# Kernel tuning notes

Hardware: AMD Instinct MI355X
Metric: run time of the kernel (lower is better)

The kernel has to match this reference:

```python
import jax, jax.numpy as jnp
import numpy as np

D_MODEL = 2048
N_HEAD = 32
N_KV_HEAD = 8
N_REP = N_HEAD // N_KV_HEAD
D_K = D_MODEL // N_HEAD
THETA = 10000.0
B, S = 2, 1024


def setup_inputs() -> dict:
    key = jax.random.key(0)
    ks = jax.random.split(key, 9)
    sd = 1.0 / np.sqrt(D_MODEL)
    return {
        "x": jax.random.normal(ks[0], (B, S, D_MODEL), jnp.float32),
        "Wq": jax.random.normal(ks[1], (D_MODEL, D_MODEL), jnp.float32) * sd,
        "bq": jax.random.normal(ks[2], (D_MODEL,), jnp.float32) * 0.02,
        "Wk": jax.random.normal(ks[3], (D_MODEL, N_KV_HEAD * D_K), jnp.float32) * sd,
        "bk": jax.random.normal(ks[4], (N_KV_HEAD * D_K,), jnp.float32) * 0.02,
        "Wv": jax.random.normal(ks[5], (D_MODEL, N_KV_HEAD * D_K), jnp.float32) * sd,
        "bv": jax.random.normal(ks[6], (N_KV_HEAD * D_K,), jnp.float32) * 0.02,
        "Wo": jax.random.normal(ks[7], (D_MODEL, D_MODEL), jnp.float32) * sd,
        "bo": jax.random.normal(ks[8], (D_MODEL,), jnp.float32) * 0.02,
    }


def _apply_rope(t, pos):
    # t: [b, h, s, d_k], pos: [s]
    half = D_K // 2
    inv_freq = 1.0 / (THETA ** (jnp.arange(half, dtype=jnp.float32) * 2.0 / D_K))
    ang = pos[:, None].astype(jnp.float32) * inv_freq[None, :]  # [s, half]
    cos = jnp.cos(ang)[None, None]  # [1,1,s,half]
    sin = jnp.sin(ang)[None, None]
    te = t[..., 0::2]
    to = t[..., 1::2]
    re = te * cos - to * sin
    ro = te * sin + to * cos
    return jnp.stack([re, ro], axis=-1).reshape(t.shape)


def reference(x, Wq, bq, Wk, bk, Wv, bv, Wo, bo):
    b, s, _ = x.shape
    q = (x @ Wq + bq).reshape(b, s, N_HEAD, D_K).transpose(0, 2, 1, 3)
    k = (x @ Wk + bk).reshape(b, s, N_KV_HEAD, D_K).transpose(0, 2, 1, 3)
    v = (x @ Wv + bv).reshape(b, s, N_KV_HEAD, D_K).transpose(0, 2, 1, 3)
    pos = jnp.arange(s)
    q = _apply_rope(q, pos)
    k = _apply_rope(k, pos)
    # GQA head repeat: [b, n_kv, s, d] -> [b, n_head, s, d]
    k = jnp.repeat(k, N_REP, axis=1)
    v = jnp.repeat(v, N_REP, axis=1)
    scores = jnp.einsum('bhnd,bhmd->bhnm', q, k) / jnp.sqrt(jnp.float32(D_K))
    mask = jnp.tril(jnp.ones((s, s), dtype=bool))
    scores = jnp.where(mask[None, None], scores, jnp.float32(-jnp.inf))
    probs = jax.nn.softmax(scores, axis=-1)
    out = jnp.einsum('bhnm,bhmd->bhnd', probs, v)
    out = out.transpose(0, 2, 1, 3).reshape(b, s, D_MODEL)
    return out @ Wo + bo
```

## Files before the change

kernel.cpp:

```cpp
#include <hip/hip_runtime.h>
#include <hip/hip_bf16.h>

#define D_MODEL 2048
#define N_HEAD 32
#define N_KV_HEAD 8
#define N_REP 4
#define D_K 64
#define S_LEN 1024
#define B_SZ 2
#define M_ROWS (B_SZ * S_LEN)
#define KV_DIM (N_KV_HEAD * D_K)
#define QKV_N 3072
#define KOFF 2048
#define VOFF 2560
#define LOG2E 1.44269504088896f

typedef __attribute__((ext_vector_type(8))) short short8;
typedef __attribute__((ext_vector_type(4))) float f32x4;

#define EXP2F(x) __builtin_amdgcn_exp2f(x)

__device__ inline unsigned short f2bf(float f) {
    union { float f; unsigned int u; } x{f};
    unsigned int r = x.u + 0x7fffu + ((x.u >> 16) & 1u);
    return (unsigned short)(r >> 16);
}
__device__ inline float bf2f(unsigned short b) {
    union { unsigned int u; float f; } x; x.u = ((unsigned int)b) << 16; return x.f;
}
__device__ inline void store_c(float* p, float v) { *p = v; }
__device__ inline void store_c(unsigned short* p, float v) { *p = f2bf(v); }

__device__ inline void load_lds16(const unsigned short* g, unsigned short* l) {
    __builtin_amdgcn_global_load_lds(
        (const __attribute__((address_space(1))) unsigned int*)g,
        (__attribute__((address_space(3))) unsigned int*)l, 16, 0, 0);
}

__global__ __launch_bounds__(256) void wprep_kernel(
        const float* __restrict__ Wq_, const float* __restrict__ Wk_,
        const float* __restrict__ Wv_, const float* __restrict__ Wo_,
        unsigned short* __restrict__ WtQKV, unsigned short* __restrict__ WtO) {
    const float* src; unsigned short* dst; int N;
    switch (blockIdx.z) {
        case 0: src = Wq_; dst = WtQKV; N = D_MODEL; break;
        case 1: src = Wk_; dst = WtQKV + (size_t)KOFF * D_MODEL; N = KV_DIM; break;
        case 2: src = Wv_; dst = WtQKV + (size_t)VOFF * D_MODEL; N = KV_DIM; break;
        default: src = Wo_; dst = WtO; N = D_MODEL; break;
    }
    int n0 = blockIdx.x * 64;
    if (n0 >= N) return;
    int k0 = blockIdx.y * 64;
    int t = threadIdx.x;
    int n = n0 + (t >> 2);
    int ks = k0 + (t & 3) * 16;
    unsigned int pk[8];
#pragma unroll
    for (int i = 0; i < 8; i++) {
        float a = src[(size_t)(ks + 2 * i) * N + n];
        float b = src[(size_t)(ks + 2 * i + 1) * N + n];
        pk[i] = (unsigned int)f2bf(a) | ((unsigned int)f2bf(b) << 16);
    }
    uint4* d = (uint4*)&dst[(size_t)n * D_MODEL + ks];
    d[0] = make_uint4(pk[0], pk[1], pk[2], pk[3]);
    d[1] = make_uint4(pk[4], pk[5], pk[6], pk[7]);
}

__global__ void cast_bf_kernel(const float* __restrict__ src,
                               unsigned short* __restrict__ dst, int n4) {
    int idx = blockIdx.x * blockDim.x + threadIdx.x;
    if (idx >= n4) return;
    float4 v = ((const float4*)src)[idx];
    unsigned int lo = (unsigned int)f2bf(v.x) | ((unsigned int)f2bf(v.y) << 16);
    unsigned int hi = (unsigned int)f2bf(v.z) | ((unsigned int)f2bf(v.w) << 16);
    ((uint2*)dst)[idx] = make_uint2(lo, hi);
}

__global__ void concat_bias_kernel(const float* __restrict__ bq, const float* __restrict__ bk,
                                   const float* __restrict__ bv, float* __restrict__ dst) {
    int i = blockIdx.x * blockDim.x + threadIdx.x;
    if (i >= QKV_N) return;
    dst[i] = (i < KOFF) ? bq[i] : (i < VOFF) ? bk[i - KOFF] : bv[i - VOFF];
}

template <typename TC>
__global__ __launch_bounds__(256) void gemm_bf16_kernel(
        const unsigned short* __restrict__ A,
        const unsigned short* __restrict__ Bt,
        const float* __restrict__ bias,
        TC* __restrict__ C, int M, int N, int K) {
    __shared__ unsigned short As[128 * 64];
    __shared__ unsigned short Bs[64 * 64];
    const int tid = threadIdx.x, lane = tid & 63;
    const int w = tid >> 6, wm = w >> 1, wn = w & 1;
    const int quad = lane >> 4, lr = lane & 15;
    const int bm = blockIdx.y * 128, bn = blockIdx.x * 64;

    f32x4 acc[4][2];
#pragma unroll
    for (int i = 0; i < 4; i++)
#pragma unroll
        for (int j = 0; j < 2; j++) acc[i][j] = (f32x4){0.f, 0.f, 0.f, 0.f};

    for (int k0 = 0; k0 < K; k0 += 64) {
        __syncthreads();
#pragma unroll
        for (int it = 0; it < 4; it++) {
            int slot = it * 256 + tid;
            int row = slot >> 3;
            int qc = (slot & 7) ^ (row & 7);
            load_lds16(A + (size_t)(bm + row) * K + k0 + qc * 8, &As[slot * 8]);
        }
#pragma unroll
        for (int it = 0; it < 2; it++) {
            int slot = it * 256 + tid;
            int row = slot >> 3;
            int qc = (slot & 7) ^ (row & 7);
            load_lds16(Bt + (size_t)(bn + row) * K + k0 + qc * 8, &Bs[slot * 8]);
        }
        __syncthreads();
#pragma unroll
        for (int ks = 0; ks < 2; ks++) {
            short8 af[4], bf[2];
#pragma unroll
            for (int i = 0; i < 4; i++) {
                int row = wm * 64 + i * 16 + lr;
                af[i] = *(const short8*)&As[(row * 8 + ((ks * 4 + quad) ^ (lr & 7))) * 8];
            }
#pragma unroll
            for (int j = 0; j < 2; j++) {
                int row = wn * 32 + j * 16 + lr;
                bf[j] = *(const short8*)&Bs[(row * 8 + ((ks * 4 + quad) ^ (lr & 7))) * 8];
            }
#pragma unroll
            for (int i = 0; i < 4; i++)
#pragma unroll
                for (int j = 0; j < 2; j++)
                    acc[i][j] = __builtin_amdgcn_mfma_f32_16x16x32_bf16(af[i], bf[j], acc[i][j], 0, 0, 0);
        }
    }
#pragma unroll
    for (int i = 0; i < 4; i++) {
#pragma unroll
        for (int j = 0; j < 2; j++) {
            int col = bn + wn * 32 + j * 16 + lr;
            int row0 = bm + wm * 64 + i * 16 + quad * 4;
            float bj = bias[col];
#pragma unroll
            for (int r = 0; r < 4; r++)
                store_c(&C[(size_t)(row0 + r) * N + col], acc[i][j][r] + bj);
        }
    }
}

__global__ void rope_bf_kernel(unsigned short* __restrict__ t) {
    const int QI = M_ROWS * N_HEAD * 32;
    const int TOT = QI + M_ROWS * N_KV_HEAD * 32;
    int idx = blockIdx.x * blockDim.x + threadIdx.x;
    if (idx >= TOT) return;
    int col_off, n_heads;
    float scale;
    if (idx < QI) { col_off = 0; n_heads = N_HEAD; scale = 0.125f * LOG2E; }
    else { idx -= QI; col_off = KOFF; n_heads = N_KV_HEAD; scale = 1.0f; }
    int i = idx & 31;
    int hh = (idx >> 5) % n_heads;
    int r = idx / (32 * n_heads);
    int s = r % S_LEN;
    float inv_freq = EXP2F((float)i * -0.41524101186f);
    float ang = (float)s * inv_freq;
    float c = __cosf(ang), sn = __sinf(ang);
    unsigned short* p = t + (size_t)r * QKV_N + col_off + hh * D_K + 2 * i;
    float te = bf2f(p[0]), to = bf2f(p[1]);
    p[0] = f2bf((te * c - to * sn) * scale);
    p[1] = f2bf((te * sn + to * c) * scale);
}

#define AST 72
struct Pre { uint4 k0, k1, v0, v1; };

__device__ __forceinline__ void issue_pre(const unsigned short* kb,
                                          const unsigned short* vb,
                                          int j0, int tid, Pre& p) {
    int f0 = tid, f1 = tid + 256;
    p.k0 = *(const uint4*)(kb + (size_t)(j0 + (f0 >> 3)) * QKV_N + (f0 & 7) * 8);
    p.k1 = *(const uint4*)(kb + (size_t)(j0 + (f1 >> 3)) * QKV_N + (f1 & 7) * 8);
    int kp = tid & 31, dg = tid >> 5;
    p.v0 = *(const uint4*)(vb + (size_t)(j0 + 2 * kp) * QKV_N + dg * 8);
    p.v1 = *(const uint4*)(vb + (size_t)(j0 + 2 * kp + 1) * QKV_N + dg * 8);
}
__device__ __forceinline__ void commit_pre(unsigned short* Ks, unsigned short* Vt,
                                           int tid, const Pre& p) {
    int f0 = tid, f1 = tid + 256;
    *(uint4*)&Ks[(f0 >> 3) * AST + (f0 & 7) * 8] = p.k0;
    *(uint4*)&Ks[(f1 >> 3) * AST + (f1 & 7) * 8] = p.k1;
    int kp = tid & 31, dg = tid >> 5;
    const unsigned short* ta = (const unsigned short*)&p.v0;
    const unsigned short* tb = (const unsigned short*)&p.v1;
#pragma unroll
    for (int i = 0; i < 8; i++) {
        unsigned int pk = (unsigned int)ta[i] | ((unsigned int)tb[i] << 16);
        *(unsigned int*)&Vt[(dg * 8 + i) * AST + 2 * kp] = pk;
    }
}

__device__ __forceinline__ void attn_tile(
        int w, int quad, int lr, bool diag,
        const unsigned short* Ks, const unsigned short* Vt, unsigned short* Ps,
        const short8* aq, f32x4* oacc, float* mrow, float* lrow) {
    f32x4 s[4];
#pragma unroll
    for (int cf = 0; cf < 4; cf++) s[cf] = (f32x4){0.f, 0.f, 0.f, 0.f};
#pragma unroll
    for (int ks = 0; ks < 2; ks++) {
#pragma unroll
        for (int cf = 0; cf < 4; cf++) {
            short8 bk = *(const short8*)&Ks[(cf * 16 + lr) * AST + ks * 32 + quad * 8];
            s[cf] = __builtin_amdgcn_mfma_f32_16x16x32_bf16(aq[ks], bk, s[cf], 0, 0, 0);
        }
    }
    if (diag) {
#pragma unroll
        for (int cf = 0; cf < 4; cf++) {
            int key = cf * 16 + lr;
#pragma unroll
            for (int r = 0; r < 4; r++)
                if (key > w * 16 + quad * 4 + r) s[cf][r] = -1e30f;
        }
    }
    float corr[4];
#pragma unroll
    for (int r = 0; r < 4; r++) {
        float rm = fmaxf(fmaxf(s[0][r], s[1][r]), fmaxf(s[2][r], s[3][r]));
        rm = fmaxf(rm, __shfl_xor(rm, 1));
        rm = fmaxf(rm, __shfl_xor(rm, 2));
        rm = fmaxf(rm, __shfl_xor(rm, 4));
        rm = fmaxf(rm, __shfl_xor(rm, 8));
        float mn = fmaxf(mrow[r], rm);
        corr[r] = EXP2F(mrow[r] - mn);
        mrow[r] = mn;
        float rs = 0.f;
#pragma unroll
        for (int cf = 0; cf < 4; cf++) {
            float p = EXP2F(s[cf][r] - mn);
            union { float f; unsigned int u; } px{p};
            px.u &= 0xFFFF0000u;
            Ps[(w * 16 + quad * 4 + r) * AST + cf * 16 + lr] =
                (unsigned short)(px.u >> 16);
            rs += px.f;
        }
        rs += __shfl_xor(rs, 1);
        rs += __shfl_xor(rs, 2);
        rs += __shfl_xor(rs, 4);
        rs += __shfl_xor(rs, 8);
        lrow[r] = lrow[r] * corr[r] + rs;
    }
#pragma unroll
    for (int cf = 0; cf < 4; cf++)
#pragma unroll
        for (int r = 0; r < 4; r++) oacc[cf][r] *= corr[r];
#pragma unroll
    for (int ks = 0; ks < 2; ks++) {
        short8 ap = *(const short8*)&Ps[(w * 16 + lr) * AST + ks * 32 + quad * 8];
#pragma unroll
        for (int cf = 0; cf < 4; cf++) {
            short8 bv = *(const short8*)&Vt[(cf * 16 + lr) * AST + ks * 32 + quad * 8];
            oacc[cf] = __builtin_amdgcn_mfma_f32_16x16x32_bf16(ap, bv, oacc[cf], 0, 0, 0);
        }
    }
}

__global__ __launch_bounds__(256) void attn_mfma_kernel(
        const unsigned short* __restrict__ qkv,
        unsigned short* __restrict__ obf) {
    __shared__ unsigned short Ks[64 * AST];
    __shared__ unsigned short Vt[64 * AST];
    __shared__ unsigned short Ps[64 * AST];
    const int tid = threadIdx.x;
    const int w = tid >> 6, lane = tid & 63;
    const int lr = lane & 15, quad = lane >> 4;
    const int h = blockIdx.y, b = blockIdx.z;
    const int kvh = h >> 2;
    const unsigned short* kb = qkv + (size_t)(b * S_LEN) * QKV_N + KOFF + kvh * D_K;
    const unsigned short* vb = qkv + (size_t)(b * S_LEN) * QKV_N + VOFF + kvh * D_K;

    const int qt = (h & 16) ? (15 - blockIdx.x) : blockIdx.x;
    const int nt = qt + 1;

    short8 aq[2];
    {
        const unsigned short* qp = qkv + (size_t)(b * S_LEN + qt * 64 + w * 16 + lr) * QKV_N
                                   + h * D_K + quad * 8;
        aq[0] = *(const short8*)qp;
        aq[1] = *(const short8*)(qp + 32);
    }
    f32x4 oacc[4];
#pragma unroll
    for (int cf = 0; cf < 4; cf++) oacc[cf] = (f32x4){0.f, 0.f, 0.f, 0.f};
    float m[4] = {-1e30f, -1e30f, -1e30f, -1e30f}, l[4] = {0.f, 0.f, 0.f, 0.f};

    Pre pre;
    issue_pre(kb, vb, 0, tid, pre);
    for (int t = 0; t < nt; t++) {
        __syncthreads();
        commit_pre(Ks, Vt, tid, pre);
        __syncthreads();
        if (t + 1 < nt) issue_pre(kb, vb, (t + 1) * 64, tid, pre);
        attn_tile(w, quad, lr, t == qt, Ks, Vt, Ps, aq, oacc, m, l);
    }
#pragma unroll
    for (int r = 0; r < 4; r++) {
        float inv = 1.f / l[r];
        int row = b * S_LEN + qt * 64 + w * 16 + quad * 4 + r;
#pragma unroll
        for (int cf = 0; cf < 4; cf++)
            obf[(size_t)row * D_MODEL + h * D_K + cf * 16 + lr] = f2bf(oacc[cf][r] * inv);
    }
}

extern "C" void kernel_launch(void* const* d_in, const int* in_sizes, int n_in,
                              void* d_out, int out_size, void* d_ws, size_t ws_size,
                              hipStream_t stream) {
    const float* x  = (const float*)d_in[0];
    const float* Wq = (const float*)d_in[1];
    const float* bq = (const float*)d_in[2];
    const float* Wk = (const float*)d_in[3];
    const float* bk = (const float*)d_in[4];
    const float* Wv = (const float*)d_in[5];
    const float* bv = (const float*)d_in[6];
    const float* Wo = (const float*)d_in[7];
    const float* bo = (const float*)d_in[8];
    float* out = (float*)d_out;

    unsigned short* xbf   = (unsigned short*)d_ws;
    unsigned short* WtQKV = xbf + (size_t)M_ROWS * D_MODEL;
    unsigned short* WtO   = WtQKV + (size_t)QKV_N * D_MODEL;
    unsigned short* qkv   = WtO + (size_t)D_MODEL * D_MODEL;
    float* bias_qkv       = (float*)(qkv + (size_t)M_ROWS * QKV_N);
    unsigned short* obf   = xbf;

    dim3 gb(256);

    cast_bf_kernel<<<(M_ROWS * D_MODEL / 4 + 255) / 256, gb, 0, stream>>>(x, xbf, M_ROWS * D_MODEL / 4);
    wprep_kernel<<<dim3(32, 32, 4), gb, 0, stream>>>(Wq, Wk, Wv, Wo, WtQKV, WtO);
    concat_bias_kernel<<<(QKV_N + 255) / 256, gb, 0, stream>>>(bq, bk, bv, bias_qkv);
    gemm_bf16_kernel<unsigned short><<<dim3(QKV_N / 64, M_ROWS / 128), gb, 0, stream>>>(
        xbf, WtQKV, bias_qkv, qkv, M_ROWS, QKV_N, D_MODEL);
    rope_bf_kernel<<<(M_ROWS * (N_HEAD + N_KV_HEAD) * 32 + 255) / 256, gb, 0, stream>>>(qkv);
    attn_mfma_kernel<<<dim3(16, N_HEAD, B_SZ), gb, 0, stream>>>(qkv, obf);
    gemm_bf16_kernel<float><<<dim3(D_MODEL / 64, M_ROWS / 128), gb, 0, stream>>>(
        obf, WtO, bo, out, M_ROWS, D_MODEL, D_MODEL);
}
```

Baseline: 234.6 us.

## Rewrite attention with 32x32x16 MFMA and register-resident P via permlane32 swaps

The attention kernel now uses 128-row query tiles (32 rows per wave) and 32x32x16 bf16 MFMAs. It computes S^T so each lane owns a single query row, which lets the softmax reductions work in registers with one permlane32 swap. P is repacked into MFMA operands with perm/permlane32_swap instead of a trip through LDS, which drops the Ps buffer. The output is staged through LDS for coalesced 16-byte stores. Waves in a block now see different causal extents, so some waves sit idle while others finish. The grid halves to 8x32x2 blocks with a batch-based tile-order flip, which lowers parallelism.

```diff
diff --git a/kernel.cpp b/kernel.cpp
--- a/kernel.cpp
+++ b/kernel.cpp
@@ -17,6 +17,7 @@
 
 typedef __attribute__((ext_vector_type(8))) short short8;
 typedef __attribute__((ext_vector_type(4))) float f32x4;
+typedef __attribute__((ext_vector_type(16))) float f32x16;
 
 #define EXP2F(x) __builtin_amdgcn_exp2f(x)
 
@@ -35,6 +36,11 @@
     __builtin_amdgcn_global_load_lds(
         (const __attribute__((address_space(1))) unsigned int*)g,
         (__attribute__((address_space(3))) unsigned int*)l, 16, 0, 0);
+}
+
+__device__ __forceinline__ unsigned int permpack(float hi_f, float lo_f) {
+    union { float f; unsigned int u; } a{hi_f}, b{lo_f};
+    return __builtin_amdgcn_perm(a.u, b.u, 0x07060302u);
 }
 
 __global__ __launch_bounds__(256) void wprep_kernel(
@@ -203,100 +209,38 @@
     }
 }
 
-__device__ __forceinline__ void attn_tile(
-        int w, int quad, int lr, bool diag,
-        const unsigned short* Ks, const unsigned short* Vt, unsigned short* Ps,
-        const short8* aq, f32x4* oacc, float* mrow, float* lrow) {
-    f32x4 s[4];
-#pragma unroll
-    for (int cf = 0; cf < 4; cf++) s[cf] = (f32x4){0.f, 0.f, 0.f, 0.f};
-#pragma unroll
-    for (int ks = 0; ks < 2; ks++) {
-#pragma unroll
-        for (int cf = 0; cf < 4; cf++) {
-            short8 bk = *(const short8*)&Ks[(cf * 16 + lr) * AST + ks * 32 + quad * 8];
-            s[cf] = __builtin_amdgcn_mfma_f32_16x16x32_bf16(aq[ks], bk, s[cf], 0, 0, 0);
-        }
-    }
-    if (diag) {
-#pragma unroll
-        for (int cf = 0; cf < 4; cf++) {
-            int key = cf * 16 + lr;
-#pragma unroll
-            for (int r = 0; r < 4; r++)
-                if (key > w * 16 + quad * 4 + r) s[cf][r] = -1e30f;
-        }
-    }
-    float corr[4];
-#pragma unroll
-    for (int r = 0; r < 4; r++) {
-        float rm = fmaxf(fmaxf(s[0][r], s[1][r]), fmaxf(s[2][r], s[3][r]));
-        rm = fmaxf(rm, __shfl_xor(rm, 1));
-        rm = fmaxf(rm, __shfl_xor(rm, 2));
-        rm = fmaxf(rm, __shfl_xor(rm, 4));
-        rm = fmaxf(rm, __shfl_xor(rm, 8));
-        float mn = fmaxf(mrow[r], rm);
-        corr[r] = EXP2F(mrow[r] - mn);
-        mrow[r] = mn;
-        float rs = 0.f;
-#pragma unroll
-        for (int cf = 0; cf < 4; cf++) {
-            float p = EXP2F(s[cf][r] - mn);
-            union { float f; unsigned int u; } px{p};
-            px.u &= 0xFFFF0000u;
-            Ps[(w * 16 + quad * 4 + r) * AST + cf * 16 + lr] =
-                (unsigned short)(px.u >> 16);
-            rs += px.f;
-        }
-        rs += __shfl_xor(rs, 1);
-        rs += __shfl_xor(rs, 2);
-        rs += __shfl_xor(rs, 4);
-        rs += __shfl_xor(rs, 8);
-        lrow[r] = lrow[r] * corr[r] + rs;
-    }
-#pragma unroll
-    for (int cf = 0; cf < 4; cf++)
-#pragma unroll
-        for (int r = 0; r < 4; r++) oacc[cf][r] *= corr[r];
-#pragma unroll
-    for (int ks = 0; ks < 2; ks++) {
-        short8 ap = *(const short8*)&Ps[(w * 16 + lr) * AST + ks * 32 + quad * 8];
-#pragma unroll
-        for (int cf = 0; cf < 4; cf++) {
-            short8 bv = *(const short8*)&Vt[(cf * 16 + lr) * AST + ks * 32 + quad * 8];
-            oacc[cf] = __builtin_amdgcn_mfma_f32_16x16x32_bf16(ap, bv, oacc[cf], 0, 0, 0);
-        }
-    }
-}
-
 __global__ __launch_bounds__(256) void attn_mfma_kernel(
         const unsigned short* __restrict__ qkv,
         unsigned short* __restrict__ obf) {
-    __shared__ unsigned short Ks[64 * AST];
-    __shared__ unsigned short Vt[64 * AST];
-    __shared__ unsigned short Ps[64 * AST];
+    __shared__ unsigned short SM[2 * 64 * AST];
+    unsigned short* Ks = SM;
+    unsigned short* Vt = SM + 64 * AST;
     const int tid = threadIdx.x;
     const int w = tid >> 6, lane = tid & 63;
-    const int lr = lane & 15, quad = lane >> 4;
+    const int lq = lane & 31, hi = lane >> 5;
+    const int hi8 = hi * 8, hi4 = hi * 4;
     const int h = blockIdx.y, b = blockIdx.z;
     const int kvh = h >> 2;
     const unsigned short* kb = qkv + (size_t)(b * S_LEN) * QKV_N + KOFF + kvh * D_K;
     const unsigned short* vb = qkv + (size_t)(b * S_LEN) * QKV_N + VOFF + kvh * D_K;
 
-    const int qt = (h & 16) ? (15 - blockIdx.x) : blockIdx.x;
-    const int nt = qt + 1;
-
-    short8 aq[2];
+    const int qt = b ? 7 - (int)blockIdx.x : (int)blockIdx.x;
+    const int nt = 2 * qt + 2;
+    const int qw0 = qt * 128 + w * 32;
+    const int qg = qw0 + lq;
+
+    short8 aq[4];
     {
-        const unsigned short* qp = qkv + (size_t)(b * S_LEN + qt * 64 + w * 16 + lr) * QKV_N
-                                   + h * D_K + quad * 8;
-        aq[0] = *(const short8*)qp;
-        aq[1] = *(const short8*)(qp + 32);
-    }
-    f32x4 oacc[4];
-#pragma unroll
-    for (int cf = 0; cf < 4; cf++) oacc[cf] = (f32x4){0.f, 0.f, 0.f, 0.f};
-    float m[4] = {-1e30f, -1e30f, -1e30f, -1e30f}, l[4] = {0.f, 0.f, 0.f, 0.f};
+        const unsigned short* qp = qkv + (size_t)(b * S_LEN + qg) * QKV_N + h * D_K + hi8;
+#pragma unroll
+        for (int st = 0; st < 4; st++) aq[st] = *(const short8*)(qp + st * 16);
+    }
+    f32x16 oacc[2];
+#pragma unroll
+    for (int dt = 0; dt < 2; dt++)
+#pragma unroll
+        for (int r = 0; r < 16; r++) oacc[dt][r] = 0.f;
+    float m = -1e30f, l = 0.f;
 
     Pre pre;
     issue_pre(kb, vb, 0, tid, pre);
@@ -305,15 +249,119 @@
         commit_pre(Ks, Vt, tid, pre);
         __syncthreads();
         if (t + 1 < nt) issue_pre(kb, vb, (t + 1) * 64, tid, pre);
-        attn_tile(w, quad, lr, t == qt, Ks, Vt, Ps, aq, oacc, m, l);
-    }
-#pragma unroll
-    for (int r = 0; r < 4; r++) {
-        float inv = 1.f / l[r];
-        int row = b * S_LEN + qt * 64 + w * 16 + quad * 4 + r;
-#pragma unroll
-        for (int cf = 0; cf < 4; cf++)
-            obf[(size_t)row * D_MODEL + h * D_K + cf * 16 + lr] = f2bf(oacc[cf][r] * inv);
+        const int t64 = t * 64;
+        if (t64 > qw0 + 31) continue;
+
+        f32x16 s0, s1;
+#pragma unroll
+        for (int r = 0; r < 16; r++) { s0[r] = 0.f; s1[r] = 0.f; }
+#pragma unroll
+        for (int st = 0; st < 4; st++) {
+            short8 k0 = *(const short8*)&Ks[lq * AST + st * 16 + hi8];
+            short8 k1 = *(const short8*)&Ks[(32 + lq) * AST + st * 16 + hi8];
+            s0 = __builtin_amdgcn_mfma_f32_32x32x16_bf16(k0, aq[st], s0, 0, 0, 0);
+            s1 = __builtin_amdgcn_mfma_f32_32x32x16_bf16(k1, aq[st], s1, 0, 0, 0);
+        }
+        float px[32];
+#pragma unroll
+        for (int r = 0; r < 16; r++) { px[r] = s0[r]; px[16 + r] = s1[r]; }
+        if (t64 + 63 > qw0) {
+#pragma unroll
+            for (int kh = 0; kh < 2; kh++)
+#pragma unroll
+                for (int r = 0; r < 16; r++) {
+                    int kg = t64 + kh * 32 + ((r & 3) + 8 * (r >> 2)) + hi4;
+                    if (kg > qg) px[kh * 16 + r] = -1e30f;
+                }
+        }
+        float tm[16];
+#pragma unroll
+        for (int i = 0; i < 16; i++) tm[i] = fmaxf(px[i], px[i + 16]);
+#pragma unroll
+        for (int i = 0; i < 8; i++) tm[i] = fmaxf(tm[i], tm[i + 8]);
+#pragma unroll
+        for (int i = 0; i < 4; i++) tm[i] = fmaxf(tm[i], tm[i + 4]);
+        float lmax = fmaxf(fmaxf(tm[0], tm[1]), fmaxf(tm[2], tm[3]));
+        union { float f; unsigned int u; } mb{lmax};
+        auto rr = __builtin_amdgcn_permlane32_swap((int)mb.u, (int)mb.u, false, false);
+        union { unsigned int u; float f; } ra, rb;
+        ra.u = (unsigned int)rr[0];
+        rb.u = (unsigned int)rr[1];
+        float mn = fmaxf(m, fmaxf(ra.f, rb.f));
+        float corr = EXP2F(m - mn);
+        m = mn;
+        float p[32], pm[32];
+#pragma unroll
+        for (int i = 0; i < 32; i++) {
+            p[i] = EXP2F(px[i] - mn);
+            union { float f; unsigned int u; } pu{p[i]};
+            pu.u &= 0xFFFF0000u;
+            pm[i] = pu.f;
+        }
+        float ts[16];
+#pragma unroll
+        for (int i = 0; i < 16; i++) ts[i] = pm[i] + pm[i + 16];
+#pragma unroll
+        for (int i = 0; i < 8; i++) ts[i] = ts[i] + ts[i + 8];
+#pragma unroll
+        for (int i = 0; i < 4; i++) ts[i] = ts[i] + ts[i + 4];
+        float lsum = (ts[0] + ts[1]) + (ts[2] + ts[3]);
+        union { float f; unsigned int u; } sb{lsum};
+        auto rr2 = __builtin_amdgcn_permlane32_swap((int)sb.u, (int)sb.u, false, false);
+        union { unsigned int u; float f; } sa2, sb2;
+        sa2.u = (unsigned int)rr2[0];
+        sb2.u = (unsigned int)rr2[1];
+        l = l * corr + (sa2.f + sb2.f);
+#pragma unroll
+        for (int dt = 0; dt < 2; dt++)
+#pragma unroll
+            for (int r = 0; r < 16; r++) oacc[dt][r] *= corr;
+        short8 pf[4];
+#pragma unroll
+        for (int kh = 0; kh < 2; kh++)
+#pragma unroll
+            for (int s = 0; s < 2; s++) {
+                int base = kh * 16 + 8 * s;
+                unsigned int a01 = permpack(p[base + 1], p[base + 0]);
+                unsigned int a23 = permpack(p[base + 3], p[base + 2]);
+                unsigned int a45 = permpack(p[base + 5], p[base + 4]);
+                unsigned int a67 = permpack(p[base + 7], p[base + 6]);
+                auto r02 = __builtin_amdgcn_permlane32_swap((int)a01, (int)a45, false, false);
+                auto r13 = __builtin_amdgcn_permlane32_swap((int)a23, (int)a67, false, false);
+                union { unsigned int wd[4]; short8 v; } pk;
+                pk.wd[0] = (unsigned int)r02[0];
+                pk.wd[1] = (unsigned int)r13[0];
+                pk.wd[2] = (unsigned int)r02[1];
+                pk.wd[3] = (unsigned int)r13[1];
+                pf[kh * 2 + s] = pk.v;
+            }
+#pragma unroll
+        for (int dt = 0; dt < 2; dt++)
+#pragma unroll
+            for (int sl = 0; sl < 4; sl++) {
+                short8 va = *(const short8*)&Vt[(dt * 32 + lq) * AST + sl * 16 + hi8];
+                oacc[dt] = __builtin_amdgcn_mfma_f32_32x32x16_bf16(va, pf[sl], oacc[dt], 0, 0, 0);
+            }
+    }
+    __syncthreads();
+    float inv = 1.f / l;
+    unsigned short* Os = SM + w * 32 * AST;
+#pragma unroll
+    for (int dt = 0; dt < 2; dt++)
+#pragma unroll
+        for (int j = 0; j < 8; j++) {
+            int d = dt * 32 + ((2 * j) & 3) + 8 * (j >> 1) + hi4;
+            unsigned int pk = (unsigned int)f2bf(oacc[dt][2 * j] * inv)
+                            | ((unsigned int)f2bf(oacc[dt][2 * j + 1] * inv) << 16);
+            *(unsigned int*)&Os[lq * AST + d] = pk;
+        }
+    __syncthreads();
+#pragma unroll
+    for (int j = 0; j < 4; j++) {
+        int row = j * 8 + (lane >> 3);
+        short8 v = *(const short8*)&Os[row * AST + (lane & 7) * 8];
+        int qrow = b * S_LEN + qw0 + row;
+        *(short8*)&obf[(size_t)qrow * D_MODEL + h * D_K + (lane & 7) * 8] = v;
     }
 }
 
@@ -346,7 +394,7 @@
     gemm_bf16_kernel<unsigned short><<<dim3(QKV_N / 64, M_ROWS / 128), gb, 0, stream>>>(
         xbf, WtQKV, bias_qkv, qkv, M_ROWS, QKV_N, D_MODEL);
     rope_bf_kernel<<<(M_ROWS * (N_HEAD + N_KV_HEAD) * 32 + 255) / 256, gb, 0, stream>>>(qkv);
-    attn_mfma_kernel<<<dim3(16, N_HEAD, B_SZ), gb, 0, stream>>>(qkv, obf);
+    attn_mfma_kernel<<<dim3(8, N_HEAD, B_SZ), gb, 0, stream>>>(qkv, obf);
     gemm_bf16_kernel<float><<<dim3(D_MODEL / 64, M_ROWS / 128), gb, 0, stream>>>(
         obf, WtO, bo, out, M_ROWS, D_MODEL, D_MODEL);
 }
```

Measured after the change: 229.0 us. -2.4%, faster.
